# Optimization experiments

Measured on AMD Instinct MI355X. Metric: run time of the kernel, lower is better.

The kernel has to match this reference:

```python
import jax, jax.numpy as jnp
import numpy as np

H = 16  # n_heads
D = 1024  # d_model
DK = 512  # d_model // compression_factor


def setup_inputs() -> dict:
    key0 = jax.random.key(0)
    ks = jax.random.split(key0, 8)
    Lq, B, Lk = 2048, 4, 1024
    query = jax.random.normal(ks[0], (Lq, B, D), dtype=jnp.float32)
    key = jax.random.normal(ks[1], (Lk, B, DK), dtype=jnp.float32)
    value = jax.random.normal(ks[2], (Lk, B, DK), dtype=jnp.float32)
    mask = jax.random.randint(ks[3], (B, Lq, Lk), 0, 2).astype(jnp.bool_)
    # learned params (torch Linear has weight (out,in); we store (in,out))
    sq = 1.0 / np.sqrt(D)
    sk = 1.0 / np.sqrt(DK)
    Wq = jax.random.uniform(ks[4], (D, H * (D // H)), jnp.float32, -sq, sq)
    Wk = jax.random.uniform(ks[5], (DK, H * (D // H)), jnp.float32, -sk, sk)
    Wv = jax.random.uniform(ks[6], (DK, H * (D // H)), jnp.float32, -sk, sk)
    Wc = jax.random.uniform(ks[7], (H * (D // H), D), jnp.float32, -sq, sq)
    return {"query": query, "key": key, "value": value, "mask": mask,
            "Wq": Wq, "Wk": Wk, "Wv": Wv, "Wc": Wc}


def reference(query, key, value, mask, Wq, Wk, Wv, Wc):
    # query: (Lq, B, D); key/value: (Lk, B, DK); mask: (B, Lq, Lk) True=masked
    Lq, B, _ = query.shape
    Lk = key.shape[0]
    Dh = D // H
    # projections (note: original forward uses `key` for both K and V via group_linear)
    q = (query @ Wq).reshape(Lq, B, H, Dh).transpose(1, 2, 0, 3)  # (B,H,Lq,Dh)
    k = (key @ Wk).reshape(Lk, B, H, Dh).transpose(1, 2, 0, 3)    # (B,H,Lk,Dh)
    v = (key @ Wv).reshape(Lk, B, H, Dh).transpose(1, 2, 0, 3)    # (B,H,Lk,Dh)
    q = q * (Dh ** -0.5)
    scores = jnp.einsum('bhqd,bhkd->bhqk', q, k)  # (B,H,Lq,Lk)
    scores = jnp.where(mask[:, None, :, :], -jnp.inf, scores)
    attn = jax.nn.softmax(scores.astype(jnp.float32), axis=-1).astype(scores.dtype)
    coverage = jnp.mean(attn, axis=1)  # (B,Lq,Lk)
    # attn_dropout is identity in eval / p=0
    out = jnp.einsum('bhqk,bhkd->bhqd', attn, v)  # (B,H,Lq,Dh)
    out = out.transpose(2, 0, 1, 3).reshape(Lq, B, H * Dh)  # (Lq,B,D)
    out = out @ Wc
    return out, coverage
```

## Files before the change

kernel.cpp:

```cpp
#include <hip/hip_runtime.h>
#include <hip/hip_bf16.h>
#include <stdint.h>

#define H_  16
#define D_  1024
#define DK_ 512
#define DH_ 64
#define LQ_ 2048
#define B_  4
#define LK_ 1024

typedef __attribute__((ext_vector_type(8))) short bf16x8_t;
typedef __attribute__((ext_vector_type(4))) unsigned short us4_t;
typedef __attribute__((ext_vector_type(4))) float fx4_t;
typedef __attribute__((ext_vector_type(4))) int ix4_t;
typedef __attribute__((ext_vector_type(2))) unsigned int u32x2_t;
typedef __attribute__((ext_vector_type(4))) unsigned int u32x4_t;

__device__ __forceinline__ unsigned short f2bf(float f) {
  unsigned int u = __builtin_bit_cast(unsigned int, f);
  u += 0x7fffu + ((u >> 16) & 1u);
  return (unsigned short)(u >> 16);
}

__device__ __forceinline__ void gld16(const void* g, void* l) {
  __builtin_amdgcn_global_load_lds((const __attribute__((address_space(1))) void*)g,
                                   (__attribute__((address_space(3))) void*)l, 16, 0, 0);
}

__global__ __launch_bounds__(256) void pre_k(const float* __restrict__ query,
    const float* __restrict__ key, const int* __restrict__ mask,
    const float* __restrict__ Wq, const float* __restrict__ Wk,
    const float* __restrict__ Wv, const float* __restrict__ Wc,
    unsigned short* __restrict__ queryb, unsigned short* __restrict__ keyb,
    unsigned int* __restrict__ mbits,
    unsigned short* __restrict__ WqT, unsigned short* __restrict__ WkT,
    unsigned short* __restrict__ WvT, unsigned short* __restrict__ WcT, float qscale) {
  __shared__ float tile[32][33];
  int bid = blockIdx.x, t = threadIdx.x;
  if (bid < 5120) {
    const float* in; unsigned short* out; float scale; int base;
    if (bid < 4096) { in = query; out = queryb; scale = qscale; base = bid; }
    else            { in = key;   out = keyb;   scale = 1.0f;   base = bid - 4096; }
    int i = (base * 256 + t) * 8;
    fx4_t a = *(const fx4_t*)(in + i);
    fx4_t b = *(const fx4_t*)(in + i + 4);
    unsigned short o[8];
    o[0] = f2bf(a[0] * scale); o[1] = f2bf(a[1] * scale);
    o[2] = f2bf(a[2] * scale); o[3] = f2bf(a[3] * scale);
    o[4] = f2bf(b[0] * scale); o[5] = f2bf(b[1] * scale);
    o[6] = f2bf(b[2] * scale); o[7] = f2bf(b[3] * scale);
    *(us4_t*)(out + i)     = *(us4_t*)&o[0];
    *(us4_t*)(out + i + 4) = *(us4_t*)&o[4];
  } else if (bid < 6144) {
    int wi = (bid - 5120) * 256 + t;
    const int* src = mask + (size_t)wi * 32;
    unsigned int bits = 0;
#pragma unroll
    for (int c = 0; c < 8; ++c) {
      ix4_t v = *(const ix4_t*)(src + c * 4);
#pragma unroll
      for (int j = 0; j < 4; ++j) bits |= (v[j] ? 1u : 0u) << (c * 4 + j);
    }
    mbits[wi] = bits;
  } else {
    int u = bid - 6144;
    int z = u >> 10, rem = u & 1023;
    const float* in; unsigned short* out; int K;
    const int N = 1024;
    if (z == 0)      { in = Wq; out = WqT; K = 1024; }
    else if (z == 1) { in = Wk; out = WkT; K = 512; }
    else if (z == 2) { in = Wv; out = WvT; K = 512; }
    else             { in = Wc; out = WcT; K = 1024; }
    int n0 = (rem & 31) * 32, k0 = (rem >> 5) * 32;
    if (k0 >= K) return;
    int r = t >> 3, c = (t & 7) * 4;
    fx4_t v = *(const fx4_t*)(in + (size_t)(k0 + r) * N + n0 + c);
    tile[r][c] = v[0]; tile[r][c + 1] = v[1]; tile[r][c + 2] = v[2]; tile[r][c + 3] = v[3];
    __syncthreads();
    us4_t o;
    o[0] = f2bf(tile[c + 0][r]); o[1] = f2bf(tile[c + 1][r]);
    o[2] = f2bf(tile[c + 2][r]); o[3] = f2bf(tile[c + 3][r]);
    *(us4_t*)(out + (size_t)(n0 + r) * K + k0 + c) = o;
  }
}

__global__ __launch_bounds__(256) void proj3_k(const unsigned short* __restrict__ queryb,
    const unsigned short* __restrict__ keyb, const unsigned short* __restrict__ WqT,
    const unsigned short* __restrict__ WkT, const unsigned short* __restrict__ WvT,
    unsigned short* __restrict__ qhm, unsigned short* __restrict__ khm,
    unsigned short* __restrict__ vbuf) {
  __shared__ unsigned short Alds[2][128 * 32];
  __shared__ unsigned short Blds[2][128 * 32];
  int bid = blockIdx.x;
  const unsigned short *A, *Bt; void* C; int M, K, mode, bx, by;
  const int N = 1024;
  if (bid < 512)      { A = queryb; Bt = WqT; C = qhm;  M = 8192; K = 1024; mode = 2; bx = bid & 63;  by = bid >> 6; }
  else if (bid < 768) { A = keyb;   Bt = WkT; C = khm;  M = 4096; K = 512;  mode = 2; bx = (bid - 512) & 31; by = (bid - 512) >> 5; }
  else                { A = keyb;   Bt = WvT; C = vbuf; M = 4096; K = 512;  mode = 1; bx = (bid - 768) & 31; by = (bid - 768) >> 5; }
  int t = threadIdx.x;
  int l = t & 63, w = t >> 6;
  int g = l >> 4, qi = l & 15;
  int wr = w >> 1, wc = w & 1;
  int m0 = bx * 128, n0 = by * 128;
  int rl = l >> 2, ul = (l & 3) ^ (rl & 3);
  const unsigned short* Ag = A + (size_t)(m0 + w * 32 + rl) * K + ul * 8;
  const unsigned short* Bg = Bt + (size_t)(n0 + w * 32 + rl) * K + ul * 8;
  int qx = qi & 3;
  fx4_t acc[4][4] = {};
  int nk = K / 32;

#define GSTAGE(PAR, KS) do { \
    gld16(Ag + (size_t)(KS) * 32,          &Alds[PAR][(w * 32) * 32]); \
    gld16(Ag + (size_t)(KS) * 32 + 16 * K, &Alds[PAR][(w * 32 + 16) * 32]); \
    gld16(Bg + (size_t)(KS) * 32,          &Blds[PAR][(w * 32) * 32]); \
    gld16(Bg + (size_t)(KS) * 32 + 16 * K, &Blds[PAR][(w * 32 + 16) * 32]); \
  } while (0)

#define GCOMP(PAR) do { \
    bf16x8_t af_[4], bf_[4]; \
    _Pragma("unroll") for (int mi = 0; mi < 4; ++mi) \
      af_[mi] = *(bf16x8_t*)&Alds[PAR][(wr * 64 + mi * 16 + qi) * 32 + ((g ^ qx) * 8)]; \
    _Pragma("unroll") for (int ni = 0; ni < 4; ++ni) \
      bf_[ni] = *(bf16x8_t*)&Blds[PAR][(wc * 64 + ni * 16 + qi) * 32 + ((g ^ qx) * 8)]; \
    _Pragma("unroll") for (int mi = 0; mi < 4; ++mi) \
      _Pragma("unroll") for (int ni = 0; ni < 4; ++ni) \
        acc[mi][ni] = __builtin_amdgcn_mfma_f32_16x16x32_bf16(af_[mi], bf_[ni], acc[mi][ni], 0, 0, 0); \
  } while (0)

  GSTAGE(0, 0);
  for (int ks = 0; ks < nk; ks += 2) {
    __syncthreads();
    if (ks + 1 < nk) GSTAGE(1, ks + 1);
    GCOMP(0);
    __syncthreads();
    if (ks + 2 < nk) GSTAGE(0, ks + 2);
    GCOMP(1);
  }
#undef GSTAGE
#undef GCOMP
#pragma unroll
  for (int mi = 0; mi < 4; ++mi)
#pragma unroll
    for (int ni = 0; ni < 4; ++ni) {
      int row = m0 + wr * 64 + mi * 16 + g * 4;
      int col = n0 + wc * 64 + ni * 16 + qi;
#pragma unroll
      for (int r = 0; r < 4; ++r) {
        if (mode == 1) ((unsigned short*)C)[(size_t)(row + r) * N + col] = f2bf(acc[mi][ni][r]);
        else {
          int m = row + r;
          int bb = m & 3, qq = m >> 2, hh = col >> 6, dd = col & 63;
          ((unsigned short*)C)[(((size_t)(bb * 16 + hh) * (M >> 2)) + qq) * 64 + dd] = f2bf(acc[mi][ni][r]);
        }
      }
    }
}

__global__ __launch_bounds__(256) void vtrans_k(const unsigned short* __restrict__ vb,
    unsigned short* __restrict__ vbT) {
  __shared__ unsigned short tile[64][72];
  int t = threadIdx.x;
  int lk0 = blockIdx.x * 64, n0 = blockIdx.y * 64, b = blockIdx.z;
  int i = t >> 2, c = (t & 3) * 16;
  const unsigned short* src = &vb[((size_t)(lk0 + i) * B_ + b) * D_ + n0 + c];
  *(bf16x8_t*)&tile[i][c]     = *(const bf16x8_t*)src;
  *(bf16x8_t*)&tile[i][c + 8] = *(const bf16x8_t*)(src + 8);
  __syncthreads();
  unsigned short o[16];
#pragma unroll
  for (int u = 0; u < 16; ++u) o[u] = tile[c + u][i];
  unsigned short* dst = &vbT[((size_t)b * D_ + n0 + i) * LK_ + lk0 + c];
  *(bf16x8_t*)&dst[0] = *(bf16x8_t*)&o[0];
  *(bf16x8_t*)&dst[8] = *(bf16x8_t*)&o[8];
}

__global__ __launch_bounds__(512, 3) void opass_k(const unsigned short* __restrict__ qhm,
    const unsigned short* __restrict__ khm, const unsigned short* __restrict__ vbT,
    const unsigned int* __restrict__ mbits, unsigned short* __restrict__ outp,
    float* __restrict__ linv) {
  __shared__ unsigned short Kt[2][64 * 64];
  __shared__ unsigned short Vt[2][64 * 64];
  int bid = blockIdx.x;
  int xcd = bid & 7, slot = bid >> 3;
  int pr = xcd * 8 + (slot >> 3);
  int qt = slot & 7;
  int b = pr >> 4, h = pr & 15;
  int bh = b * H_ + h;
  int t = threadIdx.x, w = t >> 6, l = t & 63, g = l >> 4, qi = l & 15;
  int q0 = qt * 256 + w * 32;
  int qlo = qi & 7;

  bf16x8_t qf[2][2];
#pragma unroll
  for (int s = 0; s < 2; ++s) {
    const unsigned short* qrow = qhm + ((size_t)bh * LQ_ + q0 + 16 * s + qi) * 64;
    qf[s][0] = *(const bf16x8_t*)(qrow + g * 8);
    qf[s][1] = *(const bf16x8_t*)(qrow + 32 + g * 8);
  }
  int srow = l >> 3, ssub = (l & 7) ^ srow;
  const unsigned short* kg = khm + (size_t)bh * LK_ * 64 + ssub * 8;
  const unsigned short* vg = vbT + (size_t)bh * 64 * LK_ + ssub * 8;
  const unsigned int* mr0 = mbits + ((size_t)b * LQ_ + q0 + qi) * 32;
  const unsigned int* mr1 = mr0 + 16 * 32;
  u32x4_t onesu = { 0x3F803F80u, 0x3F803F80u, 0x3F803F80u, 0x3F803F80u };
  bf16x8_t ones = __builtin_bit_cast(bf16x8_t, onesu);

#define STAGE(PAR, KT) do { \
    int rr_ = w * 8; \
    gld16(kg + (size_t)((KT) * 64 + rr_ + srow) * 64, &Kt[PAR][rr_ * 64]); \
    gld16(vg + (size_t)(rr_ + srow) * LK_ + (KT) * 64, &Vt[PAR][rr_ * 64]); \
  } while (0)

#define OCOMP(PAR, M0, M1) do { \
    unsigned short* Kc_ = Kt[PAR]; unsigned short* Vc_ = Vt[PAR]; \
    fx4_t z_ = {0.f, 0.f, 0.f, 0.f}; \
    _Pragma("unroll") for (int c_ = 0; c_ < 2; ++c_) { \
      fx4_t sa_[2][2]; \
      _Pragma("unroll") for (int kk_ = 0; kk_ < 2; ++kk_) { \
        int row_ = 32 * c_ + 16 * kk_ + qi; \
        bf16x8_t ka_ = *(bf16x8_t*)&Kc_[row_ * 64 + ((g ^ qlo) * 8)]; \
        bf16x8_t kb_ = *(bf16x8_t*)&Kc_[row_ * 64 + (((4 + g) ^ qlo) * 8)]; \
        sa_[0][kk_] = __builtin_amdgcn_mfma_f32_16x16x32_bf16(ka_, qf[0][0], z_, 0, 0, 0); \
        sa_[0][kk_] = __builtin_amdgcn_mfma_f32_16x16x32_bf16(kb_, qf[0][1], sa_[0][kk_], 0, 0, 0); \
        sa_[1][kk_] = __builtin_amdgcn_mfma_f32_16x16x32_bf16(ka_, qf[1][0], z_, 0, 0, 0); \
        sa_[1][kk_] = __builtin_amdgcn_mfma_f32_16x16x32_bf16(kb_, qf[1][1], sa_[1][kk_], 0, 0, 0); \
      } \
      unsigned int wm0_ = c_ ? (M0).y : (M0).x; \
      unsigned int wm1_ = c_ ? (M1).y : (M1).x; \
      bf16x8_t pb_[2]; \
      _Pragma("unroll") for (int s_ = 0; s_ < 2; ++s_) { \
        unsigned int wm_ = s_ ? wm1_ : wm0_; \
        float pv_[8]; \
        _Pragma("unroll") for (int r_ = 0; r_ < 4; ++r_) { \
          float a_ = __builtin_amdgcn_exp2f(sa_[s_][0][r_]); \
          float b2_ = __builtin_amdgcn_exp2f(sa_[s_][1][r_]); \
          pv_[r_]     = ((wm_ >> (4 * g + r_)) & 1u) ? 0.f : a_; \
          pv_[4 + r_] = ((wm_ >> (16 + 4 * g + r_)) & 1u) ? 0.f : b2_; \
        } \
        unsigned int w0_, w1_, w2_, w3_; \
        asm("v_cvt_pk_bf16_f32 %0, %1, %2" : "=v"(w0_) : "v"(pv_[0]), "v"(pv_[1])); \
        asm("v_cvt_pk_bf16_f32 %0, %1, %2" : "=v"(w1_) : "v"(pv_[2]), "v"(pv_[3])); \
        asm("v_cvt_pk_bf16_f32 %0, %1, %2" : "=v"(w2_) : "v"(pv_[4]), "v"(pv_[5])); \
        asm("v_cvt_pk_bf16_f32 %0, %1, %2" : "=v"(w3_) : "v"(pv_[6]), "v"(pv_[7])); \
        u32x4_t pw_ = { w0_, w1_, w2_, w3_ }; \
        pb_[s_] = __builtin_bit_cast(bf16x8_t, pw_); \
        o_l[s_] = __builtin_amdgcn_mfma_f32_16x16x32_bf16(ones, pb_[s_], o_l[s_], 0, 0, 0); \
      } \
      int wo_ = 8 * (g & 1); \
      int u0_ = (((4 * c_ + (g >> 1)) ^ qlo) << 4) + wo_; \
      int u1_ = (((4 * c_ + 2 + (g >> 1)) ^ qlo) << 4) + wo_; \
      _Pragma("unroll") for (int d_ = 0; d_ < 4; ++d_) { \
        const char* vb_ = (const char*)Vc_ + (d_ * 16 + qi) * 128; \
        u32x2_t lo_ = *(const u32x2_t*)(vb_ + u0_); \
        u32x2_t hi_ = *(const u32x2_t*)(vb_ + u1_); \
        u32x4_t vv_ = { lo_[0], lo_[1], hi_[0], hi_[1] }; \
        bf16x8_t vf_ = __builtin_bit_cast(bf16x8_t, vv_); \
        o_acc[0][d_] = __builtin_amdgcn_mfma_f32_16x16x32_bf16(vf_, pb_[0], o_acc[0][d_], 0, 0, 0); \
        o_acc[1][d_] = __builtin_amdgcn_mfma_f32_16x16x32_bf16(vf_, pb_[1], o_acc[1][d_], 0, 0, 0); \
      } \
    } \
  } while (0)

  STAGE(0, 0);
  uint2 mc0 = *(const uint2*)(mr0), mc1 = *(const uint2*)(mr1);
  uint2 mn0, mn1;
  fx4_t o_acc[2][4] = {};
  fx4_t o_l[2] = {};
  for (int tu = 0; tu < 8; ++tu) {
    int tt = 2 * tu;
    __syncthreads();
    mn0 = *(const uint2*)(mr0 + 2 * (tt + 1));
    mn1 = *(const uint2*)(mr1 + 2 * (tt + 1));
    STAGE(1, tt + 1);
    OCOMP(0, mc0, mc1);
    __syncthreads();
    if (tt + 2 < 16) {
      mc0 = *(const uint2*)(mr0 + 2 * (tt + 2));
      mc1 = *(const uint2*)(mr1 + 2 * (tt + 2));
      STAGE(0, tt + 2);
    }
    OCOMP(1, mn0, mn1);
  }
#undef STAGE
#undef OCOMP
  float iv[2] = { 1.0f / o_l[0][0], 1.0f / o_l[1][0] };
  if (g == 0) {
    linv[(size_t)bh * LQ_ + q0 + qi]      = iv[0];
    linv[(size_t)bh * LQ_ + q0 + 16 + qi] = iv[1];
  }
#pragma unroll
  for (int s = 0; s < 2; ++s)
#pragma unroll
    for (int d = 0; d < 4; ++d) {
      unsigned short pk[4];
#pragma unroll
      for (int r = 0; r < 4; ++r) pk[r] = f2bf(o_acc[s][d][r] * iv[s]);
      *(us4_t*)&outp[((size_t)(q0 + 16 * s + qi) * B_ + b) * D_ + h * DH_ + d * 16 + 4 * g] = *(us4_t*)&pk[0];
    }
}

#define NGEMM_ 512
__global__ __launch_bounds__(512) void covgem_k(const unsigned short* __restrict__ khm,
    const unsigned short* __restrict__ qhm, const unsigned int* __restrict__ mbits,
    const float* __restrict__ linv, float* __restrict__ cov,
    const unsigned short* __restrict__ outp, const unsigned short* __restrict__ WcT,
    float* __restrict__ out) {
  __shared__ unsigned short smem[2][2][128 * 64];
  int bid = blockIdx.x;
  int t = threadIdx.x, w = t >> 6, l = t & 63, g = l >> 4, qi = l & 15;

  if (bid < NGEMM_) {
    const int M = 8192, N = 1024, K = 1024;
    int bx = bid & 63, by = bid >> 6;
    int m0 = bx * 128, n0 = by * 128;
    int wr = w >> 2, wc = w & 3;
    unsigned short* AldsF = &smem[0][0][0];
    unsigned short* BldsF = &smem[0][1][0];
    int rl = l >> 2, ul = (l & 3) ^ (rl & 3);
    const unsigned short* Ag = outp + (size_t)(m0 + w * 16 + rl) * K + ul * 8;
    const unsigned short* Bg = WcT + (size_t)(n0 + w * 16 + rl) * K + ul * 8;
    int qx = qi & 3;
    fx4_t acc[4][2] = {};
    const int nk = K / 32;

#define GSTAGE8(PAR, KS) do { \
    gld16(Ag + (size_t)(KS) * 32, AldsF + (PAR) * 4096 + (w * 16) * 32); \
    gld16(Bg + (size_t)(KS) * 32, BldsF + (PAR) * 4096 + (w * 16) * 32); \
  } while (0)

#define GCOMP8(PAR) do { \
    bf16x8_t af_[4], bf_[2]; \
    _Pragma("unroll") for (int mi = 0; mi < 4; ++mi) \
      af_[mi] = *(bf16x8_t*)&AldsF[(PAR) * 4096 + (wr * 64 + mi * 16 + qi) * 32 + ((g ^ qx) * 8)]; \
    _Pragma("unroll") for (int ni = 0; ni < 2; ++ni) \
      bf_[ni] = *(bf16x8_t*)&BldsF[(PAR) * 4096 + (wc * 32 + ni * 16 + qi) * 32 + ((g ^ qx) * 8)]; \
    _Pragma("unroll") for (int mi = 0; mi < 4; ++mi) \
      _Pragma("unroll") for (int ni = 0; ni < 2; ++ni) \
        acc[mi][ni] = __builtin_amdgcn_mfma_f32_16x16x32_bf16(af_[mi], bf_[ni], acc[mi][ni], 0, 0, 0); \
  } while (0)

    GSTAGE8(0, 0);
    for (int ks = 0; ks < nk; ks += 2) {
      __syncthreads();
      if (ks + 1 < nk) GSTAGE8(1, ks + 1);
      GCOMP8(0);
      __syncthreads();
      if (ks + 2 < nk) GSTAGE8(0, ks + 2);
      GCOMP8(1);
    }
#undef GSTAGE8
#undef GCOMP8
#pragma unroll
    for (int mi = 0; mi < 4; ++mi)
#pragma unroll
      for (int ni = 0; ni < 2; ++ni) {
        int row = m0 + wr * 64 + mi * 16 + g * 4;
        int col = n0 + wc * 32 + ni * 16 + qi;
#pragma unroll
        for (int r = 0; r < 4; ++r)
          out[(size_t)(row + r) * N + col] = acc[mi][ni][r];
      }
    return;
  }

  int cid = bid - NGEMM_;
  int x = cid & 7;
  int b = x >> 1, keh = x & 1;
  int rest = cid >> 3;
  int ke = keh * 4 + (rest & 3);
  int qt = rest >> 2;
  int q0 = qt * 64;
  int wq = w >> 2, wk = w & 3;
  int qlo = qi & 7;
  int kbase = ke * 128;
  int qA = q0 + 32 * wq + qi;
  int qB = qA + 16;
  int srow = l >> 3, ssub = (l & 7) ^ srow;
  int wo = ke * 4 + wk;
  unsigned int MWA = mbits[((size_t)b * LQ_ + qA) * 32 + wo];
  unsigned int MWB = mbits[((size_t)b * LQ_ + qB) * 32 + wo];

#define CSTAGE2(PAR, HB) do { \
    _Pragma("unroll") for (int hh_ = 0; hh_ < 2; ++hh_) { \
      const unsigned short* kg_ = khm + (size_t)(b * H_ + (HB) + hh_) * LK_ * 64 + ssub * 8; \
      _Pragma("unroll") for (int i_ = 0; i_ < 2; ++i_) { \
        int rr_ = w * 16 + i_ * 8; \
        gld16(kg_ + (size_t)(kbase + rr_ + srow) * 64, &smem[PAR][hh_][rr_ * 64]); \
      } } } while (0)

#define CGLOB(HH, QF, IV) do { \
    const unsigned short* qra_ = qhm + ((size_t)(b * H_ + (HH)) * LQ_ + qA) * 64; \
    const unsigned short* qrb_ = qra_ + 16 * 64; \
    QF[0] = *(const bf16x8_t*)(qra_ + g * 8); QF[1] = *(const bf16x8_t*)(qra_ + 32 + g * 8); \
    QF[2] = *(const bf16x8_t*)(qrb_ + g * 8); QF[3] = *(const bf16x8_t*)(qrb_ + 32 + g * 8); \
    IV[0] = linv[((size_t)b * H_ + (HH)) * LQ_ + qA]; \
    IV[1] = linv[((size_t)b * H_ + (HH)) * LQ_ + qB]; \
  } while (0)

#define CCOMP(PAR, SLOT, QF, IV) do { \
    unsigned short* Kc_ = &smem[PAR][SLOT][0]; \
    fx4_t z_ = {0.f, 0.f, 0.f, 0.f}; \
    _Pragma("unroll") for (int ks = 0; ks < 2; ++ks) { \
      int row_ = wk * 32 + 16 * ks + qi; \
      bf16x8_t k0_ = *(bf16x8_t*)&Kc_[row_ * 64 + ((g ^ qlo) * 8)]; \
      bf16x8_t k1_ = *(bf16x8_t*)&Kc_[row_ * 64 + (((4 + g) ^ qlo) * 8)]; \
      __builtin_amdgcn_s_setprio(1); \
      fx4_t sA_ = __builtin_amdgcn_mfma_f32_16x16x32_bf16(k0_, QF[0], z_, 0, 0, 0); \
      sA_ = __builtin_amdgcn_mfma_f32_16x16x32_bf16(k1_, QF[1], sA_, 0, 0, 0); \
      fx4_t sB_ = __builtin_amdgcn_mfma_f32_16x16x32_bf16(k0_, QF[2], z_, 0, 0, 0); \
      sB_ = __builtin_amdgcn_mfma_f32_16x16x32_bf16(k1_, QF[3], sB_, 0, 0, 0); \
      __builtin_amdgcn_s_setprio(0); \
      int sh_ = 16 * ks + 4 * g; \
      _Pragma("unroll") for (int r_ = 0; r_ < 4; ++r_) { \
        float pA_ = __builtin_amdgcn_exp2f(sA_[r_]) * IV[0]; \
        float pB_ = __builtin_amdgcn_exp2f(sB_[r_]) * IV[1]; \
        cacc[0][ks][r_] += ((MWA >> (sh_ + r_)) & 1u) ? 0.f : pA_; \
        cacc[1][ks][r_] += ((MWB >> (sh_ + r_)) & 1u) ? 0.f : pB_; \
      } \
    } \
  } while (0)

  CSTAGE2(0, 0);
  bf16x8_t qc[4], qn[4];
  float ic[2], in_[2];
  fx4_t cacc[2][2] = {};
  CGLOB(0, qc, ic);
  for (int su = 0; su < 8; ++su) {
    __syncthreads();
    if (su + 1 < 8) CSTAGE2((su + 1) & 1, 2 * (su + 1));
    CGLOB(2 * su + 1, qn, in_);
    CCOMP(su & 1, 0, qc, ic);
    if (su + 1 < 8) CGLOB(2 * su + 2, qc, ic);
    CCOMP(su & 1, 1, qn, in_);
  }
#undef CSTAGE2
#undef CGLOB
#undef CCOMP
  int ko = kbase + wk * 32;
#pragma unroll
  for (int ks = 0; ks < 2; ++ks) {
    fx4_t wA = { cacc[0][ks][0] * 0.0625f, cacc[0][ks][1] * 0.0625f,
                 cacc[0][ks][2] * 0.0625f, cacc[0][ks][3] * 0.0625f };
    fx4_t wB = { cacc[1][ks][0] * 0.0625f, cacc[1][ks][1] * 0.0625f,
                 cacc[1][ks][2] * 0.0625f, cacc[1][ks][3] * 0.0625f };
    *(fx4_t*)(cov + ((size_t)b * LQ_ + qA) * LK_ + ko + ks * 16 + 4 * g) = wA;
    *(fx4_t*)(cov + ((size_t)b * LQ_ + qB) * LK_ + ko + ks * 16 + 4 * g) = wB;
  }
}

extern "C" void kernel_launch(void* const* d_in, const int* in_sizes, int n_in,
                              void* d_out, int out_size, void* d_ws, size_t ws_size,
                              hipStream_t stream) {
  (void)in_sizes; (void)n_in; (void)out_size; (void)ws_size;
  const float* query = (const float*)d_in[0];
  const float* key   = (const float*)d_in[1];
  const int* mask = (const int*)d_in[3];
  const float* Wq = (const float*)d_in[4];
  const float* Wk = (const float*)d_in[5];
  const float* Wv = (const float*)d_in[6];
  const float* Wc = (const float*)d_in[7];
  float* out = (float*)d_out;
  float* cov = out + (size_t)LQ_ * B_ * D_;

  char* p = (char*)d_ws;
  unsigned short* queryb = (unsigned short*)p; p += (size_t)LQ_ * B_ * D_ * 2;
  unsigned short* keyb   = (unsigned short*)p; p += (size_t)LK_ * B_ * DK_ * 2;
  unsigned short* WqT    = (unsigned short*)p; p += (size_t)D_ * D_ * 2;
  unsigned short* WkT    = (unsigned short*)p; p += (size_t)D_ * DK_ * 2;
  unsigned short* WvT    = (unsigned short*)p; p += (size_t)D_ * DK_ * 2;
  unsigned short* WcT    = (unsigned short*)p; p += (size_t)D_ * D_ * 2;
  unsigned short* qhm    = (unsigned short*)p; p += (size_t)LQ_ * B_ * D_ * 2;
  unsigned short* khm    = (unsigned short*)p; p += (size_t)LK_ * B_ * D_ * 2;
  unsigned short* vbuf   = (unsigned short*)p; p += (size_t)LK_ * B_ * D_ * 2;
  unsigned short* vbT    = (unsigned short*)p; p += (size_t)LK_ * B_ * D_ * 2;
  unsigned int*   mbits  = (unsigned int*)p;   p += (size_t)B_ * LQ_ * 32 * 4;
  float*          linv   = (float*)p;          p += (size_t)B_ * H_ * LQ_ * 4;
  unsigned short* outp   = queryb;

  const float QSCALE = 0.125f * 1.44269504088896340736f;

  pre_k<<<dim3(10240), 256, 0, stream>>>(query, key, mask, Wq, Wk, Wv, Wc,
                                         queryb, keyb, mbits, WqT, WkT, WvT, WcT, QSCALE);
  proj3_k<<<dim3(1024), 256, 0, stream>>>(queryb, keyb, WqT, WkT, WvT, qhm, khm, vbuf);
  vtrans_k<<<dim3(LK_ / 64, D_ / 64, B_), 256, 0, stream>>>(vbuf, vbT);
  opass_k<<<dim3(B_ * H_ * (LQ_ / 256)), 512, 0, stream>>>(qhm, khm, vbT, mbits, outp, linv);
  covgem_k<<<dim3(NGEMM_ + B_ * 8 * (LQ_ / 64)), 512, 0, stream>>>(khm, qhm, mbits, linv, cov,
                                                                   outp, WcT, out);
}
```

Before: 227.9 us.

## Interleave GEMM and coverage blocks and halve coverage LDS staging

The fused covgem kernel now interleaves output-projection GEMM blocks with coverage blocks (every third block is GEMM) instead of placing all GEMM blocks first, so the two workload types share CUs concurrently. The coverage path now stages one head's K tile per buffer instead of two, which halves shared memory from 64KB to 32KB and can raise occupancy. In exchange it adds a second barrier per iteration, and the heterogeneous block mix may load-balance unevenly.

After: 242.2 us. 1.06x slower.

```diff
diff --git a/kernel.cpp b/kernel.cpp
--- a/kernel.cpp
+++ b/kernel.cpp
@@ -300,23 +300,21 @@
     }
 }
 
-#define NGEMM_ 512
 __global__ __launch_bounds__(512) void covgem_k(const unsigned short* __restrict__ khm,
     const unsigned short* __restrict__ qhm, const unsigned int* __restrict__ mbits,
     const float* __restrict__ linv, float* __restrict__ cov,
     const unsigned short* __restrict__ outp, const unsigned short* __restrict__ WcT,
     float* __restrict__ out) {
-  __shared__ unsigned short smem[2][2][128 * 64];
+  __shared__ unsigned short smem[2][8192];
   int bid = blockIdx.x;
   int t = threadIdx.x, w = t >> 6, l = t & 63, g = l >> 4, qi = l & 15;
 
-  if (bid < NGEMM_) {
-    const int M = 8192, N = 1024, K = 1024;
-    int bx = bid & 63, by = bid >> 6;
+  if (bid % 3 == 0) {
+    int gid = bid / 3;
+    const int N = 1024, K = 1024;
+    int bx = gid & 63, by = gid >> 6;
     int m0 = bx * 128, n0 = by * 128;
     int wr = w >> 2, wc = w & 3;
-    unsigned short* AldsF = &smem[0][0][0];
-    unsigned short* BldsF = &smem[0][1][0];
     int rl = l >> 2, ul = (l & 3) ^ (rl & 3);
     const unsigned short* Ag = outp + (size_t)(m0 + w * 16 + rl) * K + ul * 8;
     const unsigned short* Bg = WcT + (size_t)(n0 + w * 16 + rl) * K + ul * 8;
@@ -325,16 +323,16 @@
     const int nk = K / 32;
 
 #define GSTAGE8(PAR, KS) do { \
-    gld16(Ag + (size_t)(KS) * 32, AldsF + (PAR) * 4096 + (w * 16) * 32); \
-    gld16(Bg + (size_t)(KS) * 32, BldsF + (PAR) * 4096 + (w * 16) * 32); \
+    gld16(Ag + (size_t)(KS) * 32, &smem[0][(PAR) * 4096 + (w * 16) * 32]); \
+    gld16(Bg + (size_t)(KS) * 32, &smem[1][(PAR) * 4096 + (w * 16) * 32]); \
   } while (0)
 
 #define GCOMP8(PAR) do { \
     bf16x8_t af_[4], bf_[2]; \
     _Pragma("unroll") for (int mi = 0; mi < 4; ++mi) \
-      af_[mi] = *(bf16x8_t*)&AldsF[(PAR) * 4096 + (wr * 64 + mi * 16 + qi) * 32 + ((g ^ qx) * 8)]; \
+      af_[mi] = *(bf16x8_t*)&smem[0][(PAR) * 4096 + (wr * 64 + mi * 16 + qi) * 32 + ((g ^ qx) * 8)]; \
     _Pragma("unroll") for (int ni = 0; ni < 2; ++ni) \
-      bf_[ni] = *(bf16x8_t*)&BldsF[(PAR) * 4096 + (wc * 32 + ni * 16 + qi) * 32 + ((g ^ qx) * 8)]; \
+      bf_[ni] = *(bf16x8_t*)&smem[1][(PAR) * 4096 + (wc * 32 + ni * 16 + qi) * 32 + ((g ^ qx) * 8)]; \
     _Pragma("unroll") for (int mi = 0; mi < 4; ++mi) \
       _Pragma("unroll") for (int ni = 0; ni < 2; ++ni) \
         acc[mi][ni] = __builtin_amdgcn_mfma_f32_16x16x32_bf16(af_[mi], bf_[ni], acc[mi][ni], 0, 0, 0); \
@@ -364,7 +362,7 @@
     return;
   }
 
-  int cid = bid - NGEMM_;
+  int cid = (bid / 3) * 2 + (bid % 3) - 1;
   int x = cid & 7;
   int b = x >> 1, keh = x & 1;
   int rest = cid >> 3;
@@ -381,13 +379,12 @@
   unsigned int MWA = mbits[((size_t)b * LQ_ + qA) * 32 + wo];
   unsigned int MWB = mbits[((size_t)b * LQ_ + qB) * 32 + wo];
 
-#define CSTAGE2(PAR, HB) do { \
-    _Pragma("unroll") for (int hh_ = 0; hh_ < 2; ++hh_) { \
-      const unsigned short* kg_ = khm + (size_t)(b * H_ + (HB) + hh_) * LK_ * 64 + ssub * 8; \
-      _Pragma("unroll") for (int i_ = 0; i_ < 2; ++i_) { \
-        int rr_ = w * 16 + i_ * 8; \
-        gld16(kg_ + (size_t)(kbase + rr_ + srow) * 64, &smem[PAR][hh_][rr_ * 64]); \
-      } } } while (0)
+#define CSTAGE(PAR, ST) do { \
+    const unsigned short* kg_ = khm + (size_t)(b * H_ + (ST)) * LK_ * 64 + ssub * 8; \
+    _Pragma("unroll") for (int i_ = 0; i_ < 2; ++i_) { \
+      int rr_ = w * 16 + i_ * 8; \
+      gld16(kg_ + (size_t)(kbase + rr_ + srow) * 64, &smem[PAR][rr_ * 64]); \
+    } } while (0)
 
 #define CGLOB(HH, QF, IV) do { \
     const unsigned short* qra_ = qhm + ((size_t)(b * H_ + (HH)) * LQ_ + qA) * 64; \
@@ -398,8 +395,8 @@
     IV[1] = linv[((size_t)b * H_ + (HH)) * LQ_ + qB]; \
   } while (0)
 
-#define CCOMP(PAR, SLOT, QF, IV) do { \
-    unsigned short* Kc_ = &smem[PAR][SLOT][0]; \
+#define CCOMP(PAR, QF, IV) do { \
+    unsigned short* Kc_ = &smem[PAR][0]; \
     fx4_t z_ = {0.f, 0.f, 0.f, 0.f}; \
     _Pragma("unroll") for (int ks = 0; ks < 2; ++ks) { \
       int row_ = wk * 32 + 16 * ks + qi; \
@@ -421,20 +418,22 @@
     } \
   } while (0)
 
-  CSTAGE2(0, 0);
+  CSTAGE(0, 0);
   bf16x8_t qc[4], qn[4];
   float ic[2], in_[2];
   fx4_t cacc[2][2] = {};
   CGLOB(0, qc, ic);
   for (int su = 0; su < 8; ++su) {
-    __syncthreads();
-    if (su + 1 < 8) CSTAGE2((su + 1) & 1, 2 * (su + 1));
-    CGLOB(2 * su + 1, qn, in_);
-    CCOMP(su & 1, 0, qc, ic);
-    if (su + 1 < 8) CGLOB(2 * su + 2, qc, ic);
-    CCOMP(su & 1, 1, qn, in_);
-  }
-#undef CSTAGE2
+    int st = 2 * su;
+    __syncthreads();
+    CSTAGE(1, st + 1);
+    CGLOB(st + 1, qn, in_);
+    CCOMP(0, qc, ic);
+    __syncthreads();
+    if (st + 2 < 16) { CSTAGE(0, st + 2); CGLOB(st + 2, qc, ic); }
+    CCOMP(1, qn, in_);
+  }
+#undef CSTAGE
 #undef CGLOB
 #undef CCOMP
   int ko = kbase + wk * 32;
@@ -485,6 +484,5 @@
   proj3_k<<<dim3(1024), 256, 0, stream>>>(queryb, keyb, WqT, WkT, WvT, qhm, khm, vbuf);
   vtrans_k<<<dim3(LK_ / 64, D_ / 64, B_), 256, 0, stream>>>(vbuf, vbT);
   opass_k<<<dim3(B_ * H_ * (LQ_ / 256)), 512, 0, stream>>>(qhm, khm, vbT, mbits, outp, linv);
-  covgem_k<<<dim3(NGEMM_ + B_ * 8 * (LQ_ / 64)), 512, 0, stream>>>(khm, qhm, mbits, linv, cov,
-                                                                   outp, WcT, out);
-}
+  covgem_k<<<dim3(1536), 512, 0, stream>>>(khm, qhm, mbits, linv, cov, outp, WcT, out);
+}
```
